# Performance work log

Measured on AMD Instinct MI355X. Metric: run time of the kernel, lower is better.

Reference implementation:

```python
import jax, jax.numpy as jnp
import numpy as np

N_NODES = 100000
N_EDGES = 3200000
D_FEAT = 128
N_CLASSES = 8


def setup_inputs() -> dict:
    key = jax.random.key(0)
    ks = jax.random.split(key, 8)
    x = jax.random.normal(ks[0], (N_NODES, D_FEAT), dtype=jnp.float32)
    edge_index = jax.random.randint(ks[1], (2, N_EDGES), 0, N_NODES, dtype=jnp.int64)
    W1 = jax.random.normal(ks[2], (D_FEAT, 32), dtype=jnp.float32) / np.sqrt(D_FEAT)
    b1 = jnp.zeros((32,), dtype=jnp.float32)
    W2 = jax.random.normal(ks[3], (32, 16), dtype=jnp.float32) / np.sqrt(32)
    b2 = jnp.zeros((16,), dtype=jnp.float32)
    Wc = jax.random.normal(ks[4], (16, N_CLASSES), dtype=jnp.float32) / np.sqrt(16)
    bc = jnp.zeros((N_CLASSES,), dtype=jnp.float32)
    return {"x": x, "edge_index": edge_index, "W1": W1, "b1": b1,
            "W2": W2, "b2": b2, "Wc": Wc, "bc": bc}


def _gcn_conv(h, src, dst, norm, W, b, num_nodes):
    # PyG GCNConv: linear transform, then sym-normalized scatter-add, then bias
    h = h @ W                                   # [N, out]
    msg = h[src] * norm[:, None]                # [E+N, out] gather + scale
    out = jax.ops.segment_sum(msg, dst, num_segments=num_nodes)
    return out + b


def reference(x, edge_index, W1, b1, W2, b2, Wc, bc):
    num_nodes = x.shape[0]
    loop = jnp.arange(num_nodes, dtype=edge_index.dtype)
    src = jnp.concatenate([edge_index[0], loop])  # add self-loops (PyG default)
    dst = jnp.concatenate([edge_index[1], loop])
    deg = jax.ops.segment_sum(jnp.ones_like(dst, dtype=x.dtype), dst,
                              num_segments=num_nodes)
    dinv = jnp.where(deg > 0, jax.lax.rsqrt(deg), 0.0)
    norm = dinv[src] * dinv[dst]                # symmetric normalization per edge

    h = _gcn_conv(x, src, dst, norm, W1, b1, num_nodes)
    h = jax.nn.relu(h)
    # dropout p=0.5 is identity in eval mode (training=False)
    h = _gcn_conv(h, src, dst, norm, W2, b2, num_nodes)
    h = jax.nn.relu(h)
    logits = h @ Wc + bc
    return jax.nn.log_softmax(logits, axis=1)
```

## Files before the change

kernel.cpp:

```cpp
#include <hip/hip_runtime.h>
#include <math.h>

#define N_NODES 100000
#define N_EDGES 3200000
#define D_FEAT 128
#define H1 32
#define H2 16
#define NC 8

#define NBUCK 391
#define BCAP 16384
#define EPB 4096
#define EPT 8

#define P_NODES 32
#define P_CAP 3072

typedef short s16x8 __attribute__((ext_vector_type(8)));
typedef float f32x4 __attribute__((ext_vector_type(4)));

__device__ inline unsigned short f2bf(float f) {
    unsigned int u = __float_as_uint(f);
    u += 0x7FFF + ((u >> 16) & 1);
    return (unsigned short)(u >> 16);
}
__device__ inline float bf2f(unsigned short h) {
    return __uint_as_float((unsigned int)h << 16);
}

__device__ inline int wave_scan_incl(int v, int lane) {
#pragma unroll
    for (int off = 1; off < 64; off <<= 1) {
        const int t = __shfl_up(v, off, 64);
        if (lane >= off) v += t;
    }
    return v;
}


__global__ void k_detect(const int* __restrict__ ei, const float* __restrict__ W1,
                         int* __restrict__ meta, int* __restrict__ bucket_cursor,
                         unsigned short* __restrict__ W1f) {
    __shared__ int red[256];
    int v = 0;
    for (int i = threadIdx.x; i < 1024; i += 256) v |= ei[2 * i + 1];
    red[threadIdx.x] = v;
    __syncthreads();
    for (int s = 128; s > 0; s >>= 1) {
        if (threadIdx.x < (unsigned)s) red[threadIdx.x] |= red[threadIdx.x + s];
        __syncthreads();
    }
    if (threadIdx.x == 0) meta[0] = (red[0] == 0) ? 1 : 0;
    for (int i = threadIdx.x; i < NBUCK; i += 256) bucket_cursor[i] = 0;
    for (int idx = threadIdx.x; idx < 2 * 4 * 64 * 8; idx += 256) {
        const int j    = idx & 7;
        const int lane = (idx >> 3) & 63;
        const int kk   = (idx >> 9) & 3;
        const int nt   = idx >> 11;
        const int k = kk * 32 + ((lane >> 4) << 3) + j;
        const int n = nt * 16 + (lane & 15);
        W1f[idx] = f2bf(W1[k * H1 + n]);
    }
}


__global__ __launch_bounds__(512) void k_bscatter(const int* __restrict__ ei,
                                                  const int* __restrict__ meta,
                                                  int* __restrict__ bucket_cursor,
                                                  int* __restrict__ ebuf) {
    __shared__ int hist[NBUCK];
    __shared__ int lofs[NBUCK];
    __shared__ int rank[NBUCK];
    __shared__ int gb[NBUCK];
    __shared__ int wsum[8];
    __shared__ int pay[EPB];
    __shared__ unsigned short pbk[EPB];
    const int tid = threadIdx.x;
    const int lane = tid & 63;
    const int wid = tid >> 6;
    for (int i = tid; i < NBUCK; i += 512) { hist[i] = 0; rank[i] = 0; }
    __syncthreads();
    const int e0 = blockIdx.x * EPB;
    const int n = min(EPB, N_EDGES - e0);
    const bool is64 = (meta[0] != 0);
    int rs[EPT], rd[EPT];
    if (is64) {
#pragma unroll
        for (int k = 0; k < EPT / 2; ++k) {
            const int i = 2 * (tid + k * 512);
            if (i < n) {
                const int e = e0 + i;
                const int4 s = *(const int4*)&ei[2 * e];
                const int4 d = *(const int4*)&ei[2 * N_EDGES + 2 * e];
                rs[2 * k] = s.x; rs[2 * k + 1] = s.z;
                rd[2 * k] = d.x; rd[2 * k + 1] = d.z;
                atomicAdd(&hist[d.x >> 8], 1);
                atomicAdd(&hist[d.z >> 8], 1);
            }
        }
    } else {
#pragma unroll
        for (int k = 0; k < EPT / 2; ++k) {
            const int i = 2 * (tid + k * 512);
            if (i < n) {
                const int e = e0 + i;
                const int2 s = *(const int2*)&ei[e];
                const int2 d = *(const int2*)&ei[N_EDGES + e];
                rs[2 * k] = s.x; rs[2 * k + 1] = s.y;
                rd[2 * k] = d.x; rd[2 * k + 1] = d.y;
                atomicAdd(&hist[d.x >> 8], 1);
                atomicAdd(&hist[d.y >> 8], 1);
            }
        }
    }
    __syncthreads();
    const int own = (tid < NBUCK) ? hist[tid] : 0;
    int incl = wave_scan_incl(own, lane);
    if (lane == 63) wsum[wid] = incl;
    __syncthreads();
    if (tid == 0) {
        int r = 0;
#pragma unroll
        for (int w = 0; w < 8; ++w) { const int t = wsum[w]; wsum[w] = r; r += t; }
    }
    __syncthreads();
    incl += wsum[wid];
    if (tid < NBUCK) {
        lofs[tid] = incl - own;
        if (own > 0) gb[tid] = tid * BCAP + atomicAdd(&bucket_cursor[tid], own);
    }
    __syncthreads();
#pragma unroll
    for (int k = 0; k < EPT / 2; ++k) {
        const int i = 2 * (tid + k * 512);
        if (i < n) {
#pragma unroll
            for (int j = 0; j < 2; ++j) {
                const int b = rd[2 * k + j] >> 8;
                const int p = lofs[b] + atomicAdd(&rank[b], 1);
                pay[p] = (rs[2 * k + j] << 8) | (rd[2 * k + j] & 255);
                pbk[p] = (unsigned short)b;
            }
        }
    }
    __syncthreads();
    for (int p = tid; p < n; p += 512) {
        const int b = pbk[p];
        ebuf[gb[b] + (p - lofs[b])] = pay[p];
    }
}


__global__ __launch_bounds__(512) void k_bfill2(const int* __restrict__ ebuf,
                                                const int* __restrict__ bucket_cursor,
                                                int* __restrict__ row_ptr,
                                                float* __restrict__ dinv,
                                                int* __restrict__ col_idx) {
    __shared__ int cnt[256];
    __shared__ int cur[256];
    __shared__ int wsum[8];
    __shared__ int srt[BCAP];
    __shared__ int s_wb, s_nb;
    const int b = blockIdx.x;
    const int tid = threadIdx.x;
    const int lane = tid & 63;
    const int wid = tid >> 6;
    const int own0 = (tid < NBUCK) ? bucket_cursor[tid] : 0;
    if (tid < 256) cnt[tid] = 0;
    int incl0 = wave_scan_incl(own0, lane);
    if (lane == 63) wsum[wid] = incl0;
    __syncthreads();
    if (tid == 0) {
        int r = 0;
#pragma unroll
        for (int w = 0; w < 8; ++w) { const int t = wsum[w]; wsum[w] = r; r += t; }
    }
    __syncthreads();
    incl0 += wsum[wid];
    if (tid == b) { s_wb = incl0 - own0; s_nb = own0; }
    __syncthreads();
    const int wb = s_wb;
    const int nb = s_nb;
    const int rb = b * BCAP;
    for (int i = tid; i < nb; i += 512)
        atomicAdd(&cnt[ebuf[rb + i] & 255], 1);
    __syncthreads();
    const int own = (tid < 256) ? cnt[tid] : 0;
    int incl = wave_scan_incl(own, lane);
    if (lane == 63) wsum[wid] = incl;
    __syncthreads();
    if (tid == 0) {
        int r = 0;
#pragma unroll
        for (int w = 0; w < 8; ++w) { const int t = wsum[w]; wsum[w] = r; r += t; }
    }
    __syncthreads();
    incl += wsum[wid];
    if (tid < 256) {
        const int excl = incl - own;
        const int v = (b << 8) + tid;
        if (v <= N_NODES) row_ptr[v] = wb + excl;
        if (v < N_NODES) dinv[v] = rsqrtf(1.0f + (float)own);
        cur[tid] = excl;
    }
    __syncthreads();
    for (int i = tid; i < nb; i += 512) {
        const int pk = ebuf[rb + i];
        const int slot = atomicAdd(&cur[pk & 255], 1);
        srt[slot] = pk >> 8;
    }
    __syncthreads();
    for (int i = tid; i < nb; i += 512)
        col_idx[wb + i] = srt[i];
}


__global__ __launch_bounds__(256) void k_gemm1m(const float* __restrict__ x,
                                                const unsigned short* __restrict__ W1f,
                                                const float* __restrict__ dinv,
                                                unsigned int* __restrict__ u1q) {
    __shared__ float os[4][16][33];
    const int tid = threadIdx.x;
    const int w = tid >> 6;
    const int lane = tid & 63;
    const int row0 = (blockIdx.x * 4 + w) * 16;
    const bool act = (row0 < N_NODES);
    if (act) {
        const int m = lane & 15;
        const int quad = lane >> 4;
        const s16x8* bf = (const s16x8*)W1f;
        f32x4 acc0 = {0.f, 0.f, 0.f, 0.f};
        f32x4 acc1 = {0.f, 0.f, 0.f, 0.f};
#pragma unroll
        for (int kk = 0; kk < 4; ++kk) {
            const float* xp = x + (size_t)(row0 + m) * D_FEAT + kk * 32 + quad * 8;
            const float4 p0 = ((const float4*)xp)[0];
            const float4 p1 = ((const float4*)xp)[1];
            s16x8 a;
            a[0] = (short)f2bf(p0.x); a[1] = (short)f2bf(p0.y);
            a[2] = (short)f2bf(p0.z); a[3] = (short)f2bf(p0.w);
            a[4] = (short)f2bf(p1.x); a[5] = (short)f2bf(p1.y);
            a[6] = (short)f2bf(p1.z); a[7] = (short)f2bf(p1.w);
            acc0 = __builtin_amdgcn_mfma_f32_16x16x32_bf16(a, bf[kk * 64 + lane], acc0, 0, 0, 0);
            acc1 = __builtin_amdgcn_mfma_f32_16x16x32_bf16(a, bf[(4 + kk) * 64 + lane], acc1, 0, 0, 0);
        }
#pragma unroll
        for (int r = 0; r < 4; ++r) {
            os[w][quad * 4 + r][m]      = acc0[r];
            os[w][quad * 4 + r][16 + m] = acc1[r];
        }
    }
    __syncthreads();
    if (act) {
        const int rl = lane >> 2;
        const int seg = lane & 3;
        const int row = row0 + rl;
        const float dv = dinv[row];
        const float* p = &os[w][rl][seg * 8];
        unsigned int pk0 = __builtin_amdgcn_cvt_pk_fp8_f32(p[0] * dv, p[1] * dv, 0u, false);
        pk0 = __builtin_amdgcn_cvt_pk_fp8_f32(p[2] * dv, p[3] * dv, pk0, true);
        unsigned int pk1 = __builtin_amdgcn_cvt_pk_fp8_f32(p[4] * dv, p[5] * dv, 0u, false);
        pk1 = __builtin_amdgcn_cvt_pk_fp8_f32(p[6] * dv, p[7] * dv, pk1, true);
        uint2 o; o.x = pk0; o.y = pk1;
        ((uint2*)u1q)[(size_t)row * 4 + seg] = o;
    }
}


#define ACC8(Q) do { \
    a0 += __builtin_amdgcn_cvt_f32_fp8((Q).x, 0); \
    a1 += __builtin_amdgcn_cvt_f32_fp8((Q).x, 1); \
    a2 += __builtin_amdgcn_cvt_f32_fp8((Q).x, 2); \
    a3 += __builtin_amdgcn_cvt_f32_fp8((Q).x, 3); \
    a4 += __builtin_amdgcn_cvt_f32_fp8((Q).y, 0); \
    a5 += __builtin_amdgcn_cvt_f32_fp8((Q).y, 1); \
    a6 += __builtin_amdgcn_cvt_f32_fp8((Q).y, 2); \
    a7 += __builtin_amdgcn_cvt_f32_fp8((Q).y, 3); \
} while (0)

__global__ __launch_bounds__(256) void k_pull1f(const int* __restrict__ row_ptr,
                                                const int* __restrict__ col_idx,
                                                const float* __restrict__ dinv,
                                                const unsigned int* __restrict__ u1q,
                                                const float* __restrict__ b1,
                                                const float* __restrict__ W2,
                                                unsigned int* __restrict__ u2b) {
    __shared__ float Ws[H1 * H2];
    __shared__ float hs[P_NODES][33];
    __shared__ int lidx[P_CAP];
    const int tid = threadIdx.x;
    for (int i = tid; i < H1 * H2; i += 256) Ws[i] = W2[i];
    const int v0 = blockIdx.x * P_NODES;
    const int base_off = row_ptr[v0];
    const int range = row_ptr[v0 + P_NODES] - base_off;
    const bool ovf = (range > P_CAP);
    const int stg = ovf ? 0 : range;
    for (int j = tid; j < stg; j += 256) lidx[j] = col_idx[base_off + j];
    __syncthreads();
    const int n = tid >> 3;
    const int half = (tid >> 2) & 1;
    const int lq = tid & 3;
    const int v = v0 + n;
    const uint2* base = (const uint2*)u1q;
    float a0 = 0.f, a1 = 0.f, a2 = 0.f, a3 = 0.f;
    float a4 = 0.f, a5 = 0.f, a6 = 0.f, a7 = 0.f;
    if (half == 0) {
        const uint2 q = base[(size_t)v * 4 + lq];
        a0 = __builtin_amdgcn_cvt_f32_fp8(q.x, 0);
        a1 = __builtin_amdgcn_cvt_f32_fp8(q.x, 1);
        a2 = __builtin_amdgcn_cvt_f32_fp8(q.x, 2);
        a3 = __builtin_amdgcn_cvt_f32_fp8(q.x, 3);
        a4 = __builtin_amdgcn_cvt_f32_fp8(q.y, 0);
        a5 = __builtin_amdgcn_cvt_f32_fp8(q.y, 1);
        a6 = __builtin_amdgcn_cvt_f32_fp8(q.y, 2);
        a7 = __builtin_amdgcn_cvt_f32_fp8(q.y, 3);
    }
    const int beg = row_ptr[v] - base_off;
    const int end = row_ptr[v + 1] - base_off;
    int i = beg + half;
    if (!ovf) {
        for (; i + 14 < end; i += 16) {
            const int s0 = lidx[i];
            const int s1 = lidx[i + 2];
            const int s2 = lidx[i + 4];
            const int s3 = lidx[i + 6];
            const int s4 = lidx[i + 8];
            const int s5 = lidx[i + 10];
            const int s6 = lidx[i + 12];
            const int s7 = lidx[i + 14];
            const uint2 q0 = base[(size_t)s0 * 4 + lq];
            const uint2 q1 = base[(size_t)s1 * 4 + lq];
            const uint2 q2 = base[(size_t)s2 * 4 + lq];
            const uint2 q3 = base[(size_t)s3 * 4 + lq];
            const uint2 q4 = base[(size_t)s4 * 4 + lq];
            const uint2 q5 = base[(size_t)s5 * 4 + lq];
            const uint2 q6 = base[(size_t)s6 * 4 + lq];
            const uint2 q7 = base[(size_t)s7 * 4 + lq];
            ACC8(q0); ACC8(q1); ACC8(q2); ACC8(q3);
            ACC8(q4); ACC8(q5); ACC8(q6); ACC8(q7);
        }
        for (; i + 6 < end; i += 8) {
            const int s0 = lidx[i];
            const int s1 = lidx[i + 2];
            const int s2 = lidx[i + 4];
            const int s3 = lidx[i + 6];
            const uint2 q0 = base[(size_t)s0 * 4 + lq];
            const uint2 q1 = base[(size_t)s1 * 4 + lq];
            const uint2 q2 = base[(size_t)s2 * 4 + lq];
            const uint2 q3 = base[(size_t)s3 * 4 + lq];
            ACC8(q0); ACC8(q1); ACC8(q2); ACC8(q3);
        }
        for (; i < end; i += 2) {
            const uint2 qq = base[(size_t)lidx[i] * 4 + lq];
            ACC8(qq);
        }
    } else {
        const int* gp = col_idx + base_off;
        for (; i + 14 < end; i += 16) {
            const int s0 = gp[i];
            const int s1 = gp[i + 2];
            const int s2 = gp[i + 4];
            const int s3 = gp[i + 6];
            const int s4 = gp[i + 8];
            const int s5 = gp[i + 10];
            const int s6 = gp[i + 12];
            const int s7 = gp[i + 14];
            const uint2 q0 = base[(size_t)s0 * 4 + lq];
            const uint2 q1 = base[(size_t)s1 * 4 + lq];
            const uint2 q2 = base[(size_t)s2 * 4 + lq];
            const uint2 q3 = base[(size_t)s3 * 4 + lq];
            const uint2 q4 = base[(size_t)s4 * 4 + lq];
            const uint2 q5 = base[(size_t)s5 * 4 + lq];
            const uint2 q6 = base[(size_t)s6 * 4 + lq];
            const uint2 q7 = base[(size_t)s7 * 4 + lq];
            ACC8(q0); ACC8(q1); ACC8(q2); ACC8(q3);
            ACC8(q4); ACC8(q5); ACC8(q6); ACC8(q7);
        }
        for (; i < end; i += 2) {
            const uint2 qq = base[(size_t)gp[i] * 4 + lq];
            ACC8(qq);
        }
    }
    a0 += __shfl_xor(a0, 4, 64); a1 += __shfl_xor(a1, 4, 64);
    a2 += __shfl_xor(a2, 4, 64); a3 += __shfl_xor(a3, 4, 64);
    a4 += __shfl_xor(a4, 4, 64); a5 += __shfl_xor(a5, 4, 64);
    a6 += __shfl_xor(a6, 4, 64); a7 += __shfl_xor(a7, 4, 64);
    if (half == 0) {
        const float dv = dinv[v];
        const float4 bb0 = ((const float4*)b1)[lq * 2];
        const float4 bb1 = ((const float4*)b1)[lq * 2 + 1];
        float* hp = &hs[n][lq * 8];
        hp[0] = fmaxf(fmaf(a0, dv, bb0.x), 0.0f);
        hp[1] = fmaxf(fmaf(a1, dv, bb0.y), 0.0f);
        hp[2] = fmaxf(fmaf(a2, dv, bb0.z), 0.0f);
        hp[3] = fmaxf(fmaf(a3, dv, bb0.w), 0.0f);
        hp[4] = fmaxf(fmaf(a4, dv, bb1.x), 0.0f);
        hp[5] = fmaxf(fmaf(a5, dv, bb1.y), 0.0f);
        hp[6] = fmaxf(fmaf(a6, dv, bb1.z), 0.0f);
        hp[7] = fmaxf(fmaf(a7, dv, bb1.w), 0.0f);
        if (lq == 0) hs[n][32] = dv;
    }
    __syncthreads();
    if (tid < 4 * P_NODES) {
        const int nn = tid >> 2;
        const int jq = tid & 3;
        const int vv = v0 + nn;
        const int j0 = jq * 4;
        const float dv = hs[nn][32];
        float s0 = 0.f, s1 = 0.f, s2 = 0.f, s3 = 0.f;
#pragma unroll
        for (int k = 0; k < H1; ++k) {
            const float hk = hs[nn][k];
            s0 = fmaf(hk, Ws[k * H2 + j0 + 0], s0);
            s1 = fmaf(hk, Ws[k * H2 + j0 + 1], s1);
            s2 = fmaf(hk, Ws[k * H2 + j0 + 2], s2);
            s3 = fmaf(hk, Ws[k * H2 + j0 + 3], s3);
        }
        uint2 o;
        o.x = (unsigned int)f2bf(s0 * dv) | ((unsigned int)f2bf(s1 * dv) << 16);
        o.y = (unsigned int)f2bf(s2 * dv) | ((unsigned int)f2bf(s3 * dv) << 16);
        ((uint2*)u2b)[(size_t)vv * 4 + jq] = o;
    }
}


#define ACC4(Q) do { \
    a0 += bf2f((unsigned short)(Q).x); \
    a1 += bf2f((unsigned short)((Q).x >> 16)); \
    a2 += bf2f((unsigned short)(Q).y); \
    a3 += bf2f((unsigned short)((Q).y >> 16)); \
} while (0)

__global__ __launch_bounds__(256) void k_pull2f(const int* __restrict__ row_ptr,
                                                const int* __restrict__ col_idx,
                                                const float* __restrict__ dinv,
                                                const unsigned int* __restrict__ u2b,
                                                const float* __restrict__ b2,
                                                const float* __restrict__ Wc,
                                                const float* __restrict__ bc,
                                                float* __restrict__ out) {
    __shared__ float hs[P_NODES][17];
    __shared__ float Wcs[H2 * NC];
    __shared__ float bcs[NC];
    __shared__ int lidx[P_CAP];
    const int tid = threadIdx.x;
    if (tid < H2 * NC) Wcs[tid] = Wc[tid];
    if (tid < NC) bcs[tid] = bc[tid];
    const int v0 = blockIdx.x * P_NODES;
    const int base_off = row_ptr[v0];
    const int range = row_ptr[v0 + P_NODES] - base_off;
    const bool ovf = (range > P_CAP);
    const int stg = ovf ? 0 : range;
    for (int j = tid; j < stg; j += 256) lidx[j] = col_idx[base_off + j];
    __syncthreads();
    const int n = tid >> 3;
    const int half = (tid >> 2) & 1;
    const int lq = tid & 3;
    const int v = v0 + n;
    const uint2* base = (const uint2*)u2b;
    float a0 = 0.f, a1 = 0.f, a2 = 0.f, a3 = 0.f;
    if (half == 0) {
        const uint2 q = base[(size_t)v * 4 + lq];
        a0 = bf2f((unsigned short)q.x); a1 = bf2f((unsigned short)(q.x >> 16));
        a2 = bf2f((unsigned short)q.y); a3 = bf2f((unsigned short)(q.y >> 16));
    }
    const int beg = row_ptr[v] - base_off;
    const int end = row_ptr[v + 1] - base_off;
    int i = beg + half;
    if (!ovf) {
        for (; i + 14 < end; i += 16) {
            const int s0 = lidx[i];
            const int s1 = lidx[i + 2];
            const int s2 = lidx[i + 4];
            const int s3 = lidx[i + 6];
            const int s4 = lidx[i + 8];
            const int s5 = lidx[i + 10];
            const int s6 = lidx[i + 12];
            const int s7 = lidx[i + 14];
            const uint2 q0 = base[(size_t)s0 * 4 + lq];
            const uint2 q1 = base[(size_t)s1 * 4 + lq];
            const uint2 q2 = base[(size_t)s2 * 4 + lq];
            const uint2 q3 = base[(size_t)s3 * 4 + lq];
            const uint2 q4 = base[(size_t)s4 * 4 + lq];
            const uint2 q5 = base[(size_t)s5 * 4 + lq];
            const uint2 q6 = base[(size_t)s6 * 4 + lq];
            const uint2 q7 = base[(size_t)s7 * 4 + lq];
            ACC4(q0); ACC4(q1); ACC4(q2); ACC4(q3);
            ACC4(q4); ACC4(q5); ACC4(q6); ACC4(q7);
        }
        for (; i + 6 < end; i += 8) {
            const int s0 = lidx[i];
            const int s1 = lidx[i + 2];
            const int s2 = lidx[i + 4];
            const int s3 = lidx[i + 6];
            const uint2 q0 = base[(size_t)s0 * 4 + lq];
            const uint2 q1 = base[(size_t)s1 * 4 + lq];
            const uint2 q2 = base[(size_t)s2 * 4 + lq];
            const uint2 q3 = base[(size_t)s3 * 4 + lq];
            ACC4(q0); ACC4(q1); ACC4(q2); ACC4(q3);
        }
        for (; i < end; i += 2) {
            const uint2 qq = base[(size_t)lidx[i] * 4 + lq];
            ACC4(qq);
        }
    } else {
        const int* gp = col_idx + base_off;
        for (; i + 14 < end; i += 16) {
            const int s0 = gp[i];
            const int s1 = gp[i + 2];
            const int s2 = gp[i + 4];
            const int s3 = gp[i + 6];
            const int s4 = gp[i + 8];
            const int s5 = gp[i + 10];
            const int s6 = gp[i + 12];
            const int s7 = gp[i + 14];
            const uint2 q0 = base[(size_t)s0 * 4 + lq];
            const uint2 q1 = base[(size_t)s1 * 4 + lq];
            const uint2 q2 = base[(size_t)s2 * 4 + lq];
            const uint2 q3 = base[(size_t)s3 * 4 + lq];
            const uint2 q4 = base[(size_t)s4 * 4 + lq];
            const uint2 q5 = base[(size_t)s5 * 4 + lq];
            const uint2 q6 = base[(size_t)s6 * 4 + lq];
            const uint2 q7 = base[(size_t)s7 * 4 + lq];
            ACC4(q0); ACC4(q1); ACC4(q2); ACC4(q3);
            ACC4(q4); ACC4(q5); ACC4(q6); ACC4(q7);
        }
        for (; i < end; i += 2) {
            const uint2 qq = base[(size_t)gp[i] * 4 + lq];
            ACC4(qq);
        }
    }
    a0 += __shfl_xor(a0, 4, 64); a1 += __shfl_xor(a1, 4, 64);
    a2 += __shfl_xor(a2, 4, 64); a3 += __shfl_xor(a3, 4, 64);
    if (half == 0) {
        const float dv = dinv[v];
        const float4 bb = ((const float4*)b2)[lq];
        float* hp = &hs[n][lq * 4];
        hp[0] = fmaxf(fmaf(a0, dv, bb.x), 0.0f);
        hp[1] = fmaxf(fmaf(a1, dv, bb.y), 0.0f);
        hp[2] = fmaxf(fmaf(a2, dv, bb.z), 0.0f);
        hp[3] = fmaxf(fmaf(a3, dv, bb.w), 0.0f);
    }
    __syncthreads();
    if (tid < P_NODES) {
        const int vv = v0 + tid;
        float lg[NC];
#pragma unroll
        for (int j = 0; j < NC; ++j) lg[j] = bcs[j];
#pragma unroll
        for (int k = 0; k < H2; ++k) {
            const float hk = hs[tid][k];
#pragma unroll
            for (int j = 0; j < NC; ++j)
                lg[j] = fmaf(hk, Wcs[k * NC + j], lg[j]);
        }
        float m = lg[0];
#pragma unroll
        for (int j = 1; j < NC; ++j) m = fmaxf(m, lg[j]);
        float s = 0.0f;
#pragma unroll
        for (int j = 0; j < NC; ++j) s += expf(lg[j] - m);
        const float lse = logf(s) + m;
        float4 o0, o1;
        o0.x = lg[0] - lse; o0.y = lg[1] - lse;
        o0.z = lg[2] - lse; o0.w = lg[3] - lse;
        o1.x = lg[4] - lse; o1.y = lg[5] - lse;
        o1.z = lg[6] - lse; o1.w = lg[7] - lse;
        float4* op = (float4*)(out + (size_t)vv * NC);
        op[0] = o0; op[1] = o1;
    }
}


extern "C" void kernel_launch(void* const* d_in, const int* in_sizes, int n_in,
                              void* d_out, int out_size, void* d_ws, size_t ws_size,
                              hipStream_t stream) {
    const float* x   = (const float*)d_in[0];
    const int*   ei  = (const int*)d_in[1];
    const float* W1  = (const float*)d_in[2];
    const float* b1  = (const float*)d_in[3];
    const float* W2  = (const float*)d_in[4];
    const float* b2  = (const float*)d_in[5];
    const float* Wc  = (const float*)d_in[6];
    const float* bc  = (const float*)d_in[7];
    float* out = (float*)d_out;

    int*   meta          = (int*)d_ws;
    int*   bucket_cursor = meta + 16;
    int*   bucket_base   = bucket_cursor + 512;
    int*   row_ptr       = bucket_base + 512;
    float* dinv          = (float*)(row_ptr + 100016);
    unsigned short* W1f  = (unsigned short*)(dinv + 100000);
    int*   col_idx       = (int*)W1f + 2048;
    int*   ebuf          = col_idx + 3200000;
    unsigned int* u1q    = (unsigned int*)ebuf;
    unsigned int* u2b    = (unsigned int*)(ebuf + NBUCK * BCAP);

    k_detect  <<<1, 256, 0, stream>>>(ei, W1, meta, bucket_cursor, W1f);
    k_bscatter<<<(N_EDGES + EPB - 1) / EPB, 512, 0, stream>>>(ei, meta, bucket_cursor, ebuf);
    k_bfill2  <<<NBUCK, 512, 0, stream>>>(ebuf, bucket_cursor, row_ptr, dinv, col_idx);

    k_gemm1m<<<(N_NODES + 63) / 64, 256, 0, stream>>>(x, W1f, dinv, u1q);
    k_pull1f<<<N_NODES / P_NODES, 256, 0, stream>>>(row_ptr, col_idx, dinv, u1q, b1, W2, u2b);
    k_pull2f<<<N_NODES / P_NODES, 256, 0, stream>>>(row_ptr, col_idx, dinv, u2b, b2, Wc, bc, out);
}
```

Before: 200.0 us.

## Fuse CSR bucket-sort with layer-1 pull and compute degrees via global atomics

Removes the detect and bfill kernels. Format detection and W1 conversion move into the scatter kernel, and per-node degree is now counted with global atomics during scatter so gemm1 can run before the CSR is built. The new fused kernel sorts each bucket half in LDS, writes row_ptr/col_idx for layer 2, and aggregates layer 1 directly from the LDS-sorted neighbour list. This saves launches and the round trip of col_idx for layer 1, at the cost of 3.2M global atomics on deg, each bucket's edges being read twice by two blocks, and a smaller bucket capacity that could overflow.

```diff
diff --git a/kernel.cpp b/kernel.cpp
--- a/kernel.cpp
+++ b/kernel.cpp
@@ -9,7 +9,8 @@
 #define NC 8
 
 #define NBUCK 391
-#define BCAP 16384
+#define BCAP 12288
+#define HCAP 6144
 #define EPB 4096
 #define EPT 8
 
@@ -38,51 +39,45 @@
 }
 
 
-__global__ void k_detect(const int* __restrict__ ei, const float* __restrict__ W1,
-                         int* __restrict__ meta, int* __restrict__ bucket_cursor,
-                         unsigned short* __restrict__ W1f) {
-    __shared__ int red[256];
-    int v = 0;
-    for (int i = threadIdx.x; i < 1024; i += 256) v |= ei[2 * i + 1];
-    red[threadIdx.x] = v;
-    __syncthreads();
-    for (int s = 128; s > 0; s >>= 1) {
-        if (threadIdx.x < (unsigned)s) red[threadIdx.x] |= red[threadIdx.x + s];
-        __syncthreads();
-    }
-    if (threadIdx.x == 0) meta[0] = (red[0] == 0) ? 1 : 0;
-    for (int i = threadIdx.x; i < NBUCK; i += 256) bucket_cursor[i] = 0;
-    for (int idx = threadIdx.x; idx < 2 * 4 * 64 * 8; idx += 256) {
-        const int j    = idx & 7;
-        const int lane = (idx >> 3) & 63;
-        const int kk   = (idx >> 9) & 3;
-        const int nt   = idx >> 11;
-        const int k = kk * 32 + ((lane >> 4) << 3) + j;
-        const int n = nt * 16 + (lane & 15);
-        W1f[idx] = f2bf(W1[k * H1 + n]);
-    }
-}
-
-
 __global__ __launch_bounds__(512) void k_bscatter(const int* __restrict__ ei,
-                                                  const int* __restrict__ meta,
+                                                  const float* __restrict__ W1,
                                                   int* __restrict__ bucket_cursor,
+                                                  int* __restrict__ deg,
+                                                  unsigned short* __restrict__ W1f,
                                                   int* __restrict__ ebuf) {
     __shared__ int hist[NBUCK];
     __shared__ int lofs[NBUCK];
     __shared__ int rank[NBUCK];
     __shared__ int gb[NBUCK];
     __shared__ int wsum[8];
+    __shared__ int s_is64;
     __shared__ int pay[EPB];
     __shared__ unsigned short pbk[EPB];
     const int tid = threadIdx.x;
     const int lane = tid & 63;
     const int wid = tid >> 6;
     for (int i = tid; i < NBUCK; i += 512) { hist[i] = 0; rank[i] = 0; }
+    if (tid < 64) {
+        int v = ei[2 * tid + 1];
+#pragma unroll
+        for (int off = 1; off < 64; off <<= 1) v |= __shfl_xor(v, off, 64);
+        if (tid == 0) s_is64 = (v == 0) ? 1 : 0;
+    }
+    if (blockIdx.x == 0) {
+        for (int idx = tid; idx < 2 * 4 * 64 * 8; idx += 512) {
+            const int j    = idx & 7;
+            const int ln   = (idx >> 3) & 63;
+            const int kk   = (idx >> 9) & 3;
+            const int nt   = idx >> 11;
+            const int k = kk * 32 + ((ln >> 4) << 3) + j;
+            const int n = nt * 16 + (ln & 15);
+            W1f[idx] = f2bf(W1[k * H1 + n]);
+        }
+    }
     __syncthreads();
     const int e0 = blockIdx.x * EPB;
     const int n = min(EPB, N_EDGES - e0);
-    const bool is64 = (meta[0] != 0);
+    const bool is64 = (s_is64 != 0);
     int rs[EPT], rd[EPT];
     if (is64) {
 #pragma unroll
@@ -96,6 +91,8 @@
                 rd[2 * k] = d.x; rd[2 * k + 1] = d.z;
                 atomicAdd(&hist[d.x >> 8], 1);
                 atomicAdd(&hist[d.z >> 8], 1);
+                atomicAdd(&deg[d.x], 1);
+                atomicAdd(&deg[d.z], 1);
             }
         }
     } else {
@@ -110,6 +107,8 @@
                 rd[2 * k] = d.x; rd[2 * k + 1] = d.y;
                 atomicAdd(&hist[d.x >> 8], 1);
                 atomicAdd(&hist[d.y >> 8], 1);
+                atomicAdd(&deg[d.x], 1);
+                atomicAdd(&deg[d.y], 1);
             }
         }
     }
@@ -151,73 +150,9 @@
 }
 
 
-__global__ __launch_bounds__(512) void k_bfill2(const int* __restrict__ ebuf,
-                                                const int* __restrict__ bucket_cursor,
-                                                int* __restrict__ row_ptr,
-                                                float* __restrict__ dinv,
-                                                int* __restrict__ col_idx) {
-    __shared__ int cnt[256];
-    __shared__ int cur[256];
-    __shared__ int wsum[8];
-    __shared__ int srt[BCAP];
-    __shared__ int s_wb, s_nb;
-    const int b = blockIdx.x;
-    const int tid = threadIdx.x;
-    const int lane = tid & 63;
-    const int wid = tid >> 6;
-    const int own0 = (tid < NBUCK) ? bucket_cursor[tid] : 0;
-    if (tid < 256) cnt[tid] = 0;
-    int incl0 = wave_scan_incl(own0, lane);
-    if (lane == 63) wsum[wid] = incl0;
-    __syncthreads();
-    if (tid == 0) {
-        int r = 0;
-#pragma unroll
-        for (int w = 0; w < 8; ++w) { const int t = wsum[w]; wsum[w] = r; r += t; }
-    }
-    __syncthreads();
-    incl0 += wsum[wid];
-    if (tid == b) { s_wb = incl0 - own0; s_nb = own0; }
-    __syncthreads();
-    const int wb = s_wb;
-    const int nb = s_nb;
-    const int rb = b * BCAP;
-    for (int i = tid; i < nb; i += 512)
-        atomicAdd(&cnt[ebuf[rb + i] & 255], 1);
-    __syncthreads();
-    const int own = (tid < 256) ? cnt[tid] : 0;
-    int incl = wave_scan_incl(own, lane);
-    if (lane == 63) wsum[wid] = incl;
-    __syncthreads();
-    if (tid == 0) {
-        int r = 0;
-#pragma unroll
-        for (int w = 0; w < 8; ++w) { const int t = wsum[w]; wsum[w] = r; r += t; }
-    }
-    __syncthreads();
-    incl += wsum[wid];
-    if (tid < 256) {
-        const int excl = incl - own;
-        const int v = (b << 8) + tid;
-        if (v <= N_NODES) row_ptr[v] = wb + excl;
-        if (v < N_NODES) dinv[v] = rsqrtf(1.0f + (float)own);
-        cur[tid] = excl;
-    }
-    __syncthreads();
-    for (int i = tid; i < nb; i += 512) {
-        const int pk = ebuf[rb + i];
-        const int slot = atomicAdd(&cur[pk & 255], 1);
-        srt[slot] = pk >> 8;
-    }
-    __syncthreads();
-    for (int i = tid; i < nb; i += 512)
-        col_idx[wb + i] = srt[i];
-}
-
-
 __global__ __launch_bounds__(256) void k_gemm1m(const float* __restrict__ x,
                                                 const unsigned short* __restrict__ W1f,
-                                                const float* __restrict__ dinv,
+                                                const int* __restrict__ deg,
                                                 unsigned int* __restrict__ u1q) {
     __shared__ float os[4][16][33];
     const int tid = threadIdx.x;
@@ -255,7 +190,7 @@
         const int rl = lane >> 2;
         const int seg = lane & 3;
         const int row = row0 + rl;
-        const float dv = dinv[row];
+        const float dv = rsqrtf(1.0f + (float)deg[row]);
         const float* p = &os[w][rl][seg * 8];
         unsigned int pk0 = __builtin_amdgcn_cvt_pk_fp8_f32(p[0] * dv, p[1] * dv, 0u, false);
         pk0 = __builtin_amdgcn_cvt_pk_fp8_f32(p[2] * dv, p[3] * dv, pk0, true);
@@ -278,56 +213,112 @@
     a7 += __builtin_amdgcn_cvt_f32_fp8((Q).y, 3); \
 } while (0)
 
-__global__ __launch_bounds__(256) void k_pull1f(const int* __restrict__ row_ptr,
-                                                const int* __restrict__ col_idx,
-                                                const float* __restrict__ dinv,
-                                                const unsigned int* __restrict__ u1q,
-                                                const float* __restrict__ b1,
-                                                const float* __restrict__ W2,
-                                                unsigned int* __restrict__ u2b) {
+__global__ __launch_bounds__(512) void k_fuse1(const int* __restrict__ ebuf,
+                                               const int* __restrict__ bucket_cursor,
+                                               const unsigned int* __restrict__ u1q,
+                                               const float* __restrict__ b1,
+                                               const float* __restrict__ W2,
+                                               int* __restrict__ row_ptr,
+                                               int* __restrict__ col_idx,
+                                               unsigned int* __restrict__ u2b) {
+    __shared__ int srt[HCAP];
+    __shared__ int cnt[256];
+    __shared__ int cur[256];
+    __shared__ int wsum[8];
+    __shared__ int wsum2[4];
     __shared__ float Ws[H1 * H2];
-    __shared__ float hs[P_NODES][33];
-    __shared__ int lidx[P_CAP];
+    __shared__ float hs[128][33];
+    __shared__ int s_wb, s_base, s_nh;
+    const int b = blockIdx.x >> 1;
+    const int h = blockIdx.x & 1;
     const int tid = threadIdx.x;
-    for (int i = tid; i < H1 * H2; i += 256) Ws[i] = W2[i];
-    const int v0 = blockIdx.x * P_NODES;
-    const int base_off = row_ptr[v0];
-    const int range = row_ptr[v0 + P_NODES] - base_off;
-    const bool ovf = (range > P_CAP);
-    const int stg = ovf ? 0 : range;
-    for (int j = tid; j < stg; j += 256) lidx[j] = col_idx[base_off + j];
-    __syncthreads();
-    const int n = tid >> 3;
-    const int half = (tid >> 2) & 1;
+    const int lane = tid & 63;
+    const int wid = tid >> 6;
+    if (tid < 256) cnt[tid] = 0;
+    for (int i = tid; i < H1 * H2; i += 512) Ws[i] = W2[i];
+    const int own0 = (tid < NBUCK) ? bucket_cursor[tid] : 0;
+    int incl0 = wave_scan_incl(own0, lane);
+    if (lane == 63) wsum[wid] = incl0;
+    __syncthreads();
+    if (tid == 0) {
+        int r = 0;
+#pragma unroll
+        for (int w = 0; w < 8; ++w) { const int t = wsum[w]; wsum[w] = r; r += t; }
+    }
+    __syncthreads();
+    if (tid == b) s_wb = incl0 + wsum[wid] - own0;
+    const int nb = bucket_cursor[b];
+    const int rb = b * BCAP;
+    for (int i = tid; i < nb; i += 512)
+        atomicAdd(&cnt[ebuf[rb + i] & 255], 1);
+    __syncthreads();
+    int ownc = 0, inclc = 0;
+    if (tid < 256) {
+        ownc = cnt[tid];
+        inclc = wave_scan_incl(ownc, lane);
+        if (lane == 63) wsum2[wid] = inclc;
+    }
+    __syncthreads();
+    if (tid == 0) {
+        int r = 0;
+#pragma unroll
+        for (int w = 0; w < 4; ++w) { const int t = wsum2[w]; wsum2[w] = r; r += t; }
+    }
+    __syncthreads();
+    const int wb = s_wb;
+    if (tid < 256) {
+        inclc += wsum2[wid];
+        const int excl = inclc - ownc;
+        cur[tid] = excl;
+        const int v = (b << 8) + tid;
+        if (v <= N_NODES) row_ptr[v] = wb + excl;
+    }
+    __syncthreads();
+    if (tid == 0) {
+        s_base = cur[h * 128];
+        s_nh = (h ? nb : cur[128]) - cur[h * 128];
+    }
+    __syncthreads();
+    const int base_h = s_base;
+    const int nh = s_nh;
+    for (int i = tid; i < nb; i += 512) {
+        const int pk = ebuf[rb + i];
+        const int dl = pk & 255;
+        if ((dl >> 7) == h) {
+            const int slot = atomicAdd(&cur[dl], 1);
+            srt[slot - base_h] = pk >> 8;
+        }
+    }
+    __syncthreads();
+    for (int i = tid; i < nh; i += 512)
+        col_idx[wb + base_h + i] = srt[i];
+    const int nnl = tid >> 2;
     const int lq = tid & 3;
-    const int v = v0 + n;
-    const uint2* base = (const uint2*)u1q;
-    float a0 = 0.f, a1 = 0.f, a2 = 0.f, a3 = 0.f;
-    float a4 = 0.f, a5 = 0.f, a6 = 0.f, a7 = 0.f;
-    if (half == 0) {
+    const int nn = h * 128 + nnl;
+    const int v = (b << 8) + nn;
+    if (v < N_NODES) {
+        const uint2* base = (const uint2*)u1q;
         const uint2 q = base[(size_t)v * 4 + lq];
-        a0 = __builtin_amdgcn_cvt_f32_fp8(q.x, 0);
-        a1 = __builtin_amdgcn_cvt_f32_fp8(q.x, 1);
-        a2 = __builtin_amdgcn_cvt_f32_fp8(q.x, 2);
-        a3 = __builtin_amdgcn_cvt_f32_fp8(q.x, 3);
-        a4 = __builtin_amdgcn_cvt_f32_fp8(q.y, 0);
-        a5 = __builtin_amdgcn_cvt_f32_fp8(q.y, 1);
-        a6 = __builtin_amdgcn_cvt_f32_fp8(q.y, 2);
-        a7 = __builtin_amdgcn_cvt_f32_fp8(q.y, 3);
-    }
-    const int beg = row_ptr[v] - base_off;
-    const int end = row_ptr[v + 1] - base_off;
-    int i = beg + half;
-    if (!ovf) {
-        for (; i + 14 < end; i += 16) {
-            const int s0 = lidx[i];
-            const int s1 = lidx[i + 2];
-            const int s2 = lidx[i + 4];
-            const int s3 = lidx[i + 6];
-            const int s4 = lidx[i + 8];
-            const int s5 = lidx[i + 10];
-            const int s6 = lidx[i + 12];
-            const int s7 = lidx[i + 14];
+        float a0 = __builtin_amdgcn_cvt_f32_fp8(q.x, 0);
+        float a1 = __builtin_amdgcn_cvt_f32_fp8(q.x, 1);
+        float a2 = __builtin_amdgcn_cvt_f32_fp8(q.x, 2);
+        float a3 = __builtin_amdgcn_cvt_f32_fp8(q.x, 3);
+        float a4 = __builtin_amdgcn_cvt_f32_fp8(q.y, 0);
+        float a5 = __builtin_amdgcn_cvt_f32_fp8(q.y, 1);
+        float a6 = __builtin_amdgcn_cvt_f32_fp8(q.y, 2);
+        float a7 = __builtin_amdgcn_cvt_f32_fp8(q.y, 3);
+        const int cn = cnt[nn];
+        const int e = cur[nn] - base_h;
+        int j = e - cn;
+        for (; j + 7 < e; j += 8) {
+            const int s0 = srt[j + 0];
+            const int s1 = srt[j + 1];
+            const int s2 = srt[j + 2];
+            const int s3 = srt[j + 3];
+            const int s4 = srt[j + 4];
+            const int s5 = srt[j + 5];
+            const int s6 = srt[j + 6];
+            const int s7 = srt[j + 7];
             const uint2 q0 = base[(size_t)s0 * 4 + lq];
             const uint2 q1 = base[(size_t)s1 * 4 + lq];
             const uint2 q2 = base[(size_t)s2 * 4 + lq];
@@ -339,57 +330,25 @@
             ACC8(q0); ACC8(q1); ACC8(q2); ACC8(q3);
             ACC8(q4); ACC8(q5); ACC8(q6); ACC8(q7);
         }
-        for (; i + 6 < end; i += 8) {
-            const int s0 = lidx[i];
-            const int s1 = lidx[i + 2];
-            const int s2 = lidx[i + 4];
-            const int s3 = lidx[i + 6];
+        for (; j + 3 < e; j += 4) {
+            const int s0 = srt[j + 0];
+            const int s1 = srt[j + 1];
+            const int s2 = srt[j + 2];
+            const int s3 = srt[j + 3];
             const uint2 q0 = base[(size_t)s0 * 4 + lq];
             const uint2 q1 = base[(size_t)s1 * 4 + lq];
             const uint2 q2 = base[(size_t)s2 * 4 + lq];
             const uint2 q3 = base[(size_t)s3 * 4 + lq];
             ACC8(q0); ACC8(q1); ACC8(q2); ACC8(q3);
         }
-        for (; i < end; i += 2) {
-            const uint2 qq = base[(size_t)lidx[i] * 4 + lq];
+        for (; j < e; ++j) {
+            const uint2 qq = base[(size_t)srt[j] * 4 + lq];
             ACC8(qq);
         }
-    } else {
-        const int* gp = col_idx + base_off;
-        for (; i + 14 < end; i += 16) {
-            const int s0 = gp[i];
-            const int s1 = gp[i + 2];
-            const int s2 = gp[i + 4];
-            const int s3 = gp[i + 6];
-            const int s4 = gp[i + 8];
-            const int s5 = gp[i + 10];
-            const int s6 = gp[i + 12];
-            const int s7 = gp[i + 14];
-            const uint2 q0 = base[(size_t)s0 * 4 + lq];
-            const uint2 q1 = base[(size_t)s1 * 4 + lq];
-            const uint2 q2 = base[(size_t)s2 * 4 + lq];
-            const uint2 q3 = base[(size_t)s3 * 4 + lq];
-            const uint2 q4 = base[(size_t)s4 * 4 + lq];
-            const uint2 q5 = base[(size_t)s5 * 4 + lq];
-            const uint2 q6 = base[(size_t)s6 * 4 + lq];
-            const uint2 q7 = base[(size_t)s7 * 4 + lq];
-            ACC8(q0); ACC8(q1); ACC8(q2); ACC8(q3);
-            ACC8(q4); ACC8(q5); ACC8(q6); ACC8(q7);
-        }
-        for (; i < end; i += 2) {
-            const uint2 qq = base[(size_t)gp[i] * 4 + lq];
-            ACC8(qq);
-        }
-    }
-    a0 += __shfl_xor(a0, 4, 64); a1 += __shfl_xor(a1, 4, 64);
-    a2 += __shfl_xor(a2, 4, 64); a3 += __shfl_xor(a3, 4, 64);
-    a4 += __shfl_xor(a4, 4, 64); a5 += __shfl_xor(a5, 4, 64);
-    a6 += __shfl_xor(a6, 4, 64); a7 += __shfl_xor(a7, 4, 64);
-    if (half == 0) {
-        const float dv = dinv[v];
+        const float dv = rsqrtf(1.0f + (float)cn);
         const float4 bb0 = ((const float4*)b1)[lq * 2];
         const float4 bb1 = ((const float4*)b1)[lq * 2 + 1];
-        float* hp = &hs[n][lq * 8];
+        float* hp = &hs[nnl][lq * 8];
         hp[0] = fmaxf(fmaf(a0, dv, bb0.x), 0.0f);
         hp[1] = fmaxf(fmaf(a1, dv, bb0.y), 0.0f);
         hp[2] = fmaxf(fmaf(a2, dv, bb0.z), 0.0f);
@@ -398,28 +357,30 @@
         hp[5] = fmaxf(fmaf(a5, dv, bb1.y), 0.0f);
         hp[6] = fmaxf(fmaf(a6, dv, bb1.z), 0.0f);
         hp[7] = fmaxf(fmaf(a7, dv, bb1.w), 0.0f);
-        if (lq == 0) hs[n][32] = dv;
-    }
-    __syncthreads();
-    if (tid < 4 * P_NODES) {
-        const int nn = tid >> 2;
+        if (lq == 0) hs[nnl][32] = dv;
+    }
+    __syncthreads();
+    {
+        const int nn2 = tid >> 2;
         const int jq = tid & 3;
-        const int vv = v0 + nn;
-        const int j0 = jq * 4;
-        const float dv = hs[nn][32];
-        float s0 = 0.f, s1 = 0.f, s2 = 0.f, s3 = 0.f;
-#pragma unroll
-        for (int k = 0; k < H1; ++k) {
-            const float hk = hs[nn][k];
-            s0 = fmaf(hk, Ws[k * H2 + j0 + 0], s0);
-            s1 = fmaf(hk, Ws[k * H2 + j0 + 1], s1);
-            s2 = fmaf(hk, Ws[k * H2 + j0 + 2], s2);
-            s3 = fmaf(hk, Ws[k * H2 + j0 + 3], s3);
-        }
-        uint2 o;
-        o.x = (unsigned int)f2bf(s0 * dv) | ((unsigned int)f2bf(s1 * dv) << 16);
-        o.y = (unsigned int)f2bf(s2 * dv) | ((unsigned int)f2bf(s3 * dv) << 16);
-        ((uint2*)u2b)[(size_t)vv * 4 + jq] = o;
+        const int v2 = (b << 8) + h * 128 + nn2;
+        if (v2 < N_NODES) {
+            const int j0 = jq * 4;
+            const float dv = hs[nn2][32];
+            float s0 = 0.f, s1 = 0.f, s2 = 0.f, s3 = 0.f;
+#pragma unroll
+            for (int k = 0; k < H1; ++k) {
+                const float hk = hs[nn2][k];
+                s0 = fmaf(hk, Ws[k * H2 + j0 + 0], s0);
+                s1 = fmaf(hk, Ws[k * H2 + j0 + 1], s1);
+                s2 = fmaf(hk, Ws[k * H2 + j0 + 2], s2);
+                s3 = fmaf(hk, Ws[k * H2 + j0 + 3], s3);
+            }
+            uint2 o;
+            o.x = (unsigned int)f2bf(s0 * dv) | ((unsigned int)f2bf(s1 * dv) << 16);
+            o.y = (unsigned int)f2bf(s2 * dv) | ((unsigned int)f2bf(s3 * dv) << 16);
+            ((uint2*)u2b)[(size_t)v2 * 4 + jq] = o;
+        }
     }
 }
 
@@ -433,7 +394,7 @@
 
 __global__ __launch_bounds__(256) void k_pull2f(const int* __restrict__ row_ptr,
                                                 const int* __restrict__ col_idx,
-                                                const float* __restrict__ dinv,
+                                                const int* __restrict__ deg,
                                                 const unsigned int* __restrict__ u2b,
                                                 const float* __restrict__ b2,
                                                 const float* __restrict__ Wc,
@@ -533,7 +494,7 @@
     a0 += __shfl_xor(a0, 4, 64); a1 += __shfl_xor(a1, 4, 64);
     a2 += __shfl_xor(a2, 4, 64); a3 += __shfl_xor(a3, 4, 64);
     if (half == 0) {
-        const float dv = dinv[v];
+        const float dv = rsqrtf(1.0f + (float)deg[v]);
         const float4 bb = ((const float4*)b2)[lq];
         float* hp = &hs[n][lq * 4];
         hp[0] = fmaxf(fmaf(a0, dv, bb.x), 0.0f);
@@ -585,22 +546,18 @@
     const float* bc  = (const float*)d_in[7];
     float* out = (float*)d_out;
 
-    int*   meta          = (int*)d_ws;
-    int*   bucket_cursor = meta + 16;
-    int*   bucket_base   = bucket_cursor + 512;
-    int*   row_ptr       = bucket_base + 512;
-    float* dinv          = (float*)(row_ptr + 100016);
-    unsigned short* W1f  = (unsigned short*)(dinv + 100000);
-    int*   col_idx       = (int*)W1f + 2048;
-    int*   ebuf          = col_idx + 3200000;
-    unsigned int* u1q    = (unsigned int*)ebuf;
-    unsigned int* u2b    = (unsigned int*)(ebuf + NBUCK * BCAP);
-
-    k_detect  <<<1, 256, 0, stream>>>(ei, W1, meta, bucket_cursor, W1f);
-    k_bscatter<<<(N_EDGES + EPB - 1) / EPB, 512, 0, stream>>>(ei, meta, bucket_cursor, ebuf);
-    k_bfill2  <<<NBUCK, 512, 0, stream>>>(ebuf, bucket_cursor, row_ptr, dinv, col_idx);
-
-    k_gemm1m<<<(N_NODES + 63) / 64, 256, 0, stream>>>(x, W1f, dinv, u1q);
-    k_pull1f<<<N_NODES / P_NODES, 256, 0, stream>>>(row_ptr, col_idx, dinv, u1q, b1, W2, u2b);
-    k_pull2f<<<N_NODES / P_NODES, 256, 0, stream>>>(row_ptr, col_idx, dinv, u2b, b2, Wc, bc, out);
-}
+    int*   bucket_cursor = (int*)d_ws;
+    int*   deg           = bucket_cursor + 512;
+    unsigned short* W1f  = (unsigned short*)(deg + 100000);
+    int*   row_ptr       = (int*)W1f + 2048;
+    int*   col_idx       = row_ptr + 100016;
+    unsigned int* u1q    = (unsigned int*)(col_idx + 3200000);
+    unsigned int* u2b    = u1q + 800000;
+    int*   ebuf          = (int*)(u2b + 800000);
+
+    hipMemsetAsync(bucket_cursor, 0, (512 + 100000) * sizeof(int), stream);
+    k_bscatter<<<(N_EDGES + EPB - 1) / EPB, 512, 0, stream>>>(ei, W1, bucket_cursor, deg, W1f, ebuf);
+    k_gemm1m<<<(N_NODES + 63) / 64, 256, 0, stream>>>(x, W1f, deg, u1q);
+    k_fuse1 <<<NBUCK * 2, 512, 0, stream>>>(ebuf, bucket_cursor, u1q, b1, W2, row_ptr, col_idx, u2b);
+    k_pull2f<<<N_NODES / P_NODES, 256, 0, stream>>>(row_ptr, col_idx, deg, u2b, b2, Wc, bc, out);
+}
```

Measured after the change: 318.3 us. 59.2% more time.
